# Optimization experiments

Hardware: AMD Instinct MI355X
Metric: run time of the kernel (lower is better)

Reference implementation:

```python
import jax, jax.numpy as jnp
import numpy as np

IN_C, OUT_C = 128, 256
KH, KW = 3, 3
STRIDE = (1, 1)
PAD = (1, 1)


def setup_inputs() -> dict:
    key = jax.random.key(0)
    kx, kw = jax.random.split(key)
    x = jax.random.normal(kx, (32, IN_C, 56, 56), dtype=jnp.float32)
    k = 1.0 / (IN_C * KH * KW)
    weight = (2.0 * jax.random.uniform(kw, (OUT_C, IN_C, KH, KW), dtype=jnp.float32) - 1.0) * (k ** 0.5)
    return {"x": x, "weight": weight}


def reference(x, weight):
    # Equivalent to the as_strided broadcast-multiply-sum: a plain 2D cross-correlation
    # (no bias), NCHW input, OIHW weight, stride (1,1), padding (1,1).
    return jax.lax.conv_general_dilated(
        x, weight,
        window_strides=STRIDE,
        padding=[(PAD[0], PAD[0]), (PAD[1], PAD[1])],
        dimension_numbers=("NCHW", "OIHW", "NCHW"),
    )
```

## Files before the change

### kernel.cpp

```cpp
#include <hip/hip_runtime.h>

typedef __attribute__((ext_vector_type(8))) short short8;
typedef __attribute__((ext_vector_type(4))) float floatx4;

#define IN_C 128
#define OUT_C 256
#define NB 32
#define HW 56
#define S_PER_N (HW * HW)
#define M_TOTAL (NB * S_PER_N)
#define PH 58
#define PW 66
#define XN_ELEMS (NB * PH * PW * IN_C)
#define WT_ELEMS (9 * OUT_C * IN_C)
#define XF_BLOCKS (PH * NB)
#define WF_BLOCKS (WT_ELEMS / 256)

__device__ __forceinline__ unsigned short f2bf(float f) {
    unsigned int u = __builtin_bit_cast(unsigned int, f);
    u = (u + 0x7FFFu + ((u >> 16) & 1u)) >> 16;
    return (unsigned short)u;
}

__device__ __forceinline__ void gld_lds16(const unsigned short* g, unsigned short* l) {
    __builtin_amdgcn_global_load_lds(
        (const __attribute__((address_space(1))) unsigned int*)g,
        (__attribute__((address_space(3))) unsigned int*)l, 16, 0, 0);
}

__global__ void xform_all(const float* __restrict__ x, const float* __restrict__ w,
                          unsigned short* __restrict__ xn, unsigned short* __restrict__ wt) {
    const int bid = blockIdx.x;
    const int tid = threadIdx.x;

    if (bid >= XF_BLOCKS) {
        const int idx = (bid - XF_BLOCKS) * 256 + tid;
        const int ic  = idx & 127;
        const int oc  = (idx >> 7) & 255;
        const int khw = idx >> 15;
        wt[idx] = f2bf(w[(oc * IN_C + ic) * 9 + khw]);
        return;
    }

    const int ihp = bid % PH;
    const int n   = bid / PH;
    unsigned int* __restrict__ row32 =
        (unsigned int*)(xn + (size_t)(n * PH + ihp) * PW * IN_C);
    const int WORDS = PW * IN_C / 2;

    if (ihp == 0 || ihp == PH - 1) {
        for (int i = tid; i < WORDS; i += 256) row32[i] = 0u;
        return;
    }
    if (tid < 128) {
        int p = (tid >> 6) * (PW - 1);
        row32[p * 64 + (tid & 63)] = 0u;
    }
    const int ih = ihp - 1;
    const float* __restrict__ xrow = x + (size_t)n * IN_C * S_PER_N + (size_t)ih * HW;
#pragma unroll
    for (int t = 0; t < 4; ++t) {
        const int item = tid + t * 256;
        if (item >= 64 * 14) break;
        const int icw  = item & 63;
        const int pix4 = item >> 6;
        const float4 v0 = *(const float4*)(xrow + (size_t)(2 * icw)     * S_PER_N + pix4 * 4);
        const float4 v1 = *(const float4*)(xrow + (size_t)(2 * icw + 1) * S_PER_N + pix4 * 4);
        unsigned int* o = row32 + (pix4 * 4 + 1) * 64 + icw;
        o[0]   = (unsigned int)f2bf(v0.x) | ((unsigned int)f2bf(v1.x) << 16);
        o[64]  = (unsigned int)f2bf(v0.y) | ((unsigned int)f2bf(v1.y) << 16);
        o[128] = (unsigned int)f2bf(v0.z) | ((unsigned int)f2bf(v1.z) << 16);
        o[192] = (unsigned int)f2bf(v0.w) | ((unsigned int)f2bf(v1.w) << 16);
    }
}

__global__ void __launch_bounds__(256, 3)
conv_mfma(const unsigned short* __restrict__ xn,
          const unsigned short* __restrict__ wt,
          float* __restrict__ out) {
    const int tid  = threadIdx.x;
    const int lane = tid & 63;
    const int wv   = tid >> 6;
    const int l15  = lane & 15;
    const int quad = lane >> 4;

    const int bx0 = blockIdx.x;
    const int bx  = (bx0 & 7) * 196 + (bx0 >> 3);
    const int tile_oc = bx & 1;
    const int tile_m  = bx >> 1;

    const int s_blk  = tile_m * 128;
    const int oc_blk = tile_oc * 128;
    const int s0  = s_blk + (wv & 1) * 64;
    const int oc0 = oc_blk + (wv >> 1) * 64;

    __shared__ unsigned short A_lds[128 * 64];
    __shared__ unsigned short B_lds[128 * 64];

    const int srow = tid >> 3;
    const int sic  = ((tid & 7) ^ (srow & 7)) * 8;

    const unsigned short* a_g[4];
    const unsigned short* b_g[4];
#pragma unroll
    for (int q = 0; q < 4; ++q) {
        int row = q * 32 + srow;
        a_g[q] = wt + (size_t)(oc_blk + row) * IN_C + sic;
        int sg = s_blk + row;
        int n  = sg / S_PER_N;
        int r  = sg % S_PER_N;
        int oh = r / HW, ow = r % HW;
        b_g[q] = xn + (size_t)((n * PH + oh) * PW + ow) * IN_C + sic;
    }
    unsigned short* a_l = A_lds + tid * 8;
    unsigned short* b_l = B_lds + tid * 8;

    const int fr7 = l15 & 7;
    int afo[4], bfo[4];
#pragma unroll
    for (int i = 0; i < 4; ++i)
        afo[i] = ((wv >> 1) * 64 + i * 16 + l15) * 64 + ((quad ^ fr7) * 8);
#pragma unroll
    for (int j = 0; j < 4; ++j)
        bfo[j] = ((wv & 1) * 64 + j * 16 + l15) * 64 + ((quad ^ fr7) * 8);

    floatx4 acc[4][4];
#pragma unroll
    for (int i = 0; i < 4; ++i)
#pragma unroll
        for (int j = 0; j < 4; ++j) acc[i][j] = (floatx4){0.f, 0.f, 0.f, 0.f};

#pragma unroll
    for (int khw = 0; khw < 9; ++khw) {
        const int xo = ((khw / 3) * PW + (khw % 3)) * IN_C;
        const int wo = khw * OUT_C * IN_C;
#pragma unroll
        for (int h = 0; h < 2; ++h) {
            const int ic0 = h * 64;
            __syncthreads();
#pragma unroll
            for (int q = 0; q < 4; ++q) {
                gld_lds16(a_g[q] + wo + ic0, a_l + q * 2048);
                gld_lds16(b_g[q] + xo + ic0, b_l + q * 2048);
            }
            __syncthreads();

#pragma unroll
            for (int kk = 0; kk < 2; ++kk) {
                const int ko = kk * 32;
                short8 a[4], b[4];
#pragma unroll
                for (int i = 0; i < 4; ++i) a[i] = *(const short8*)(A_lds + (afo[i] ^ ko));
#pragma unroll
                for (int j = 0; j < 4; ++j) b[j] = *(const short8*)(B_lds + (bfo[j] ^ ko));
#pragma unroll
                for (int i = 0; i < 4; ++i)
#pragma unroll
                    for (int j = 0; j < 4; ++j)
                        acc[i][j] = __builtin_amdgcn_mfma_f32_16x16x32_bf16(
                            a[i], b[j], acc[i][j], 0, 0, 0);
            }
        }
    }

#pragma unroll
    for (int j = 0; j < 4; ++j) {
        int s_glob = s0 + j * 16 + l15;
        int n = s_glob / S_PER_N;
        int s = s_glob % S_PER_N;
        float* obase = out + (size_t)n * OUT_C * S_PER_N + s;
#pragma unroll
        for (int i = 0; i < 4; ++i) {
            int oc = oc0 + i * 16 + quad * 4;
#pragma unroll
            for (int r = 0; r < 4; ++r)
                obase[(size_t)(oc + r) * S_PER_N] = acc[i][j][r];
        }
    }
}

extern "C" void kernel_launch(void* const* d_in, const int* in_sizes, int n_in,
                              void* d_out, int out_size, void* d_ws, size_t ws_size,
                              hipStream_t stream) {
    const float* x = (const float*)d_in[0];
    const float* w = (const float*)d_in[1];
    float* out = (float*)d_out;

    unsigned short* xn = (unsigned short*)d_ws;
    unsigned short* wt = xn + XN_ELEMS;

    xform_all<<<XF_BLOCKS + WF_BLOCKS, 256, 0, stream>>>(x, w, xn, wt);
    conv_mfma<<<(M_TOTAL / 128) * 2, 256, 0, stream>>>(xn, wt, out);
}
```

Before: 203.6 us.

## Enlarge conv GEMM tile to all 256 output channels per block

Each block now computes all 256 output channels for 128 spatial positions instead of splitting channels across two blocks. Each wave holds an 8x4 grid of MFMA accumulators, so the input patch loaded into LDS is reused across twice as many channels and is no longer fetched by two separate blocks. The cost is double the accumulator registers and a larger A tile in LDS. Occupancy drops (launch bounds 3 to 2 blocks per CU), there are half as many blocks, and the swizzle over 784 blocks changes.

```diff
diff --git a/kernel.cpp b/kernel.cpp
--- a/kernel.cpp
+++ b/kernel.cpp
@@ -74,59 +74,55 @@
     }
 }
 
-__global__ void __launch_bounds__(256, 3)
+__global__ void __launch_bounds__(256, 2)
 conv_mfma(const unsigned short* __restrict__ xn,
           const unsigned short* __restrict__ wt,
           float* __restrict__ out) {
     const int tid  = threadIdx.x;
     const int lane = tid & 63;
     const int wv   = tid >> 6;
+    const int ws   = wv & 1;
+    const int wo_  = wv >> 1;
     const int l15  = lane & 15;
     const int quad = lane >> 4;
+    const int fr7  = l15 & 7;
 
-    const int bx0 = blockIdx.x;
-    const int bx  = (bx0 & 7) * 196 + (bx0 >> 3);
-    const int tile_oc = bx & 1;
-    const int tile_m  = bx >> 1;
+    const int bx0    = blockIdx.x;
+    const int tile_m = (bx0 & 7) * 98 + (bx0 >> 3);
+    const int s_blk  = tile_m * 128;
 
-    const int s_blk  = tile_m * 128;
-    const int oc_blk = tile_oc * 128;
-    const int s0  = s_blk + (wv & 1) * 64;
-    const int oc0 = oc_blk + (wv >> 1) * 64;
-
-    __shared__ unsigned short A_lds[128 * 64];
+    __shared__ unsigned short A_lds[256 * 64];
     __shared__ unsigned short B_lds[128 * 64];
 
     const int srow = tid >> 3;
     const int sic  = ((tid & 7) ^ (srow & 7)) * 8;
 
-    const unsigned short* a_g[4];
+    const unsigned short* a_g[8];
     const unsigned short* b_g[4];
 #pragma unroll
-    for (int q = 0; q < 4; ++q) {
-        int row = q * 32 + srow;
-        a_g[q] = wt + (size_t)(oc_blk + row) * IN_C + sic;
-        int sg = s_blk + row;
+    for (int g = 0; g < 8; ++g)
+        a_g[g] = wt + (size_t)(g * 32 + srow) * IN_C + sic;
+#pragma unroll
+    for (int g = 0; g < 4; ++g) {
+        int sg = s_blk + g * 32 + srow;
         int n  = sg / S_PER_N;
         int r  = sg % S_PER_N;
         int oh = r / HW, ow = r % HW;
-        b_g[q] = xn + (size_t)((n * PH + oh) * PW + ow) * IN_C + sic;
+        b_g[g] = xn + (size_t)((n * PH + oh) * PW + ow) * IN_C + sic;
     }
-    unsigned short* a_l = A_lds + tid * 8;
-    unsigned short* b_l = B_lds + tid * 8;
 
-    const int fr7 = l15 & 7;
-    int afo[4], bfo[4];
+    const int slot = (quad ^ fr7) * 8;
+    int afo[8], bfo[4];
 #pragma unroll
-    for (int i = 0; i < 4; ++i)
-        afo[i] = ((wv >> 1) * 64 + i * 16 + l15) * 64 + ((quad ^ fr7) * 8);
+    for (int i = 0; i < 8; ++i)
+        afo[i] = (wo_ * 128 + i * 16 + l15) * 64 + slot;
 #pragma unroll
     for (int j = 0; j < 4; ++j)
-        bfo[j] = ((wv & 1) * 64 + j * 16 + l15) * 64 + ((quad ^ fr7) * 8);
+        bfo[j] = (ws * 64 + j * 16 + l15) * 64 + slot;
 
-    floatx4 acc[4][4];
+    floatx4 acc[8][4];
 #pragma unroll
-    for (int i = 0; i < 4; ++i)
+    for (int i = 0; i < 8; ++i)
 #pragma unroll
         for (int j = 0; j < 4; ++j) acc[i][j] = (floatx4){0.f, 0.f, 0.f, 0.f};
 
@@ -139,22 +135,23 @@
             const int ic0 = h * 64;
             __syncthreads();
 #pragma unroll
-            for (int q = 0; q < 4; ++q) {
-                gld_lds16(a_g[q] + wo + ic0, a_l + q * 2048);
-                gld_lds16(b_g[q] + xo + ic0, b_l + q * 2048);
-            }
+            for (int g = 0; g < 8; ++g)
+                gld_lds16(a_g[g] + wo + ic0, A_lds + g * 2048 + tid * 8);
+#pragma unroll
+            for (int g = 0; g < 4; ++g)
+                gld_lds16(b_g[g] + xo + ic0, B_lds + g * 2048 + tid * 8);
             __syncthreads();
 
 #pragma unroll
             for (int kk = 0; kk < 2; ++kk) {
                 const int ko = kk * 32;
-                short8 a[4], b[4];
+                short8 a[8], b[4];
 #pragma unroll
-                for (int i = 0; i < 4; ++i) a[i] = *(const short8*)(A_lds + (afo[i] ^ ko));
+                for (int i = 0; i < 8; ++i) a[i] = *(const short8*)(A_lds + (afo[i] ^ ko));
 #pragma unroll
                 for (int j = 0; j < 4; ++j) b[j] = *(const short8*)(B_lds + (bfo[j] ^ ko));
 #pragma unroll
-                for (int i = 0; i < 4; ++i)
+                for (int i = 0; i < 8; ++i)
 #pragma unroll
                     for (int j = 0; j < 4; ++j)
                         acc[i][j] = __builtin_amdgcn_mfma_f32_16x16x32_bf16(
@@ -163,6 +160,8 @@
         }
     }
 
+    const int s0  = s_blk + ws * 64;
+    const int oc0 = wo_ * 128;
 #pragma unroll
     for (int j = 0; j < 4; ++j) {
         int s_glob = s0 + j * 16 + l15;
@@ -170,7 +169,7 @@
         int s = s_glob % S_PER_N;
         float* obase = out + (size_t)n * OUT_C * S_PER_N + s;
 #pragma unroll
-        for (int i = 0; i < 4; ++i) {
+        for (int i = 0; i < 8; ++i) {
             int oc = oc0 + i * 16 + quad * 4;
 #pragma unroll
             for (int r = 0; r < 4; ++r)
@@ -190,5 +189,5 @@
     unsigned short* wt = xn + XN_ELEMS;
 
     xform_all<<<XF_BLOCKS + WF_BLOCKS, 256, 0, stream>>>(x, w, xn, wt);
-    conv_mfma<<<(M_TOTAL / 128) * 2, 256, 0, stream>>>(xn, wt, out);
+    conv_mfma<<<M_TOTAL / 128, 256, 0, stream>>>(xn, wt, out);
 }
```

New measurement: 209.0 us. 1.03x slower.

## Double-buffer LDS tiles to overlap global loads with MFMA compute

Applied to the files above, without the earlier changes.

Splits A and B shared tiles into two buffers and prefetches the next K-slice with direct global-to-LDS loads while MFMAs consume the current one. One barrier per step replaces the previous two. LDS use doubles to 64 KB per block and launch bounds drop to 2 blocks per CU, which lowers occupancy. The barrier placement after the waitcnt must still stop the writes to the next buffer from racing with reads of the old one.

```diff
diff --git a/kernel.cpp b/kernel.cpp
--- a/kernel.cpp
+++ b/kernel.cpp
@@ -74,7 +74,7 @@
     }
 }
 
-__global__ void __launch_bounds__(256, 3)
+__global__ void __launch_bounds__(256, 2)
 conv_mfma(const unsigned short* __restrict__ xn,
           const unsigned short* __restrict__ wt,
           float* __restrict__ out) {
@@ -83,6 +83,7 @@
     const int wv   = tid >> 6;
     const int l15  = lane & 15;
     const int quad = lane >> 4;
+    const int fr7  = l15 & 7;
 
     const int bx0 = blockIdx.x;
     const int bx  = (bx0 & 7) * 196 + (bx0 >> 3);
@@ -94,8 +95,8 @@
     const int s0  = s_blk + (wv & 1) * 64;
     const int oc0 = oc_blk + (wv >> 1) * 64;
 
-    __shared__ unsigned short A_lds[128 * 64];
-    __shared__ unsigned short B_lds[128 * 64];
+    __shared__ unsigned short A_lds[2][128 * 64];
+    __shared__ unsigned short B_lds[2][128 * 64];
 
     const int srow = tid >> 3;
     const int sic  = ((tid & 7) ^ (srow & 7)) * 8;
@@ -112,17 +113,15 @@
         int oh = r / HW, ow = r % HW;
         b_g[q] = xn + (size_t)((n * PH + oh) * PW + ow) * IN_C + sic;
     }
-    unsigned short* a_l = A_lds + tid * 8;
-    unsigned short* b_l = B_lds + tid * 8;
-
-    const int fr7 = l15 & 7;
+
+    const int slot = (quad ^ fr7) * 8;
     int afo[4], bfo[4];
 #pragma unroll
     for (int i = 0; i < 4; ++i)
-        afo[i] = ((wv >> 1) * 64 + i * 16 + l15) * 64 + ((quad ^ fr7) * 8);
+        afo[i] = ((wv >> 1) * 64 + i * 16 + l15) * 64 + slot;
 #pragma unroll
     for (int j = 0; j < 4; ++j)
-        bfo[j] = ((wv & 1) * 64 + j * 16 + l15) * 64 + ((quad ^ fr7) * 8);
+        bfo[j] = ((wv & 1) * 64 + j * 16 + l15) * 64 + slot;
 
     floatx4 acc[4][4];
 #pragma unroll
@@ -131,36 +130,44 @@
         for (int j = 0; j < 4; ++j) acc[i][j] = (floatx4){0.f, 0.f, 0.f, 0.f};
 
 #pragma unroll
-    for (int khw = 0; khw < 9; ++khw) {
-        const int xo = ((khw / 3) * PW + (khw % 3)) * IN_C;
-        const int wo = khw * OUT_C * IN_C;
-#pragma unroll
-        for (int h = 0; h < 2; ++h) {
-            const int ic0 = h * 64;
-            __syncthreads();
+    for (int q = 0; q < 4; ++q) {
+        gld_lds16(a_g[q], &A_lds[0][q * 2048 + tid * 8]);
+        gld_lds16(b_g[q], &B_lds[0][q * 2048 + tid * 8]);
+    }
+    asm volatile("s_waitcnt vmcnt(0)" ::: "memory");
+    __builtin_amdgcn_s_barrier();
+
+#pragma unroll
+    for (int t = 0; t < 18; ++t) {
+        const int c = t & 1;
+        if (t < 17) {
+            const int tn   = t + 1;
+            const int khwn = tn >> 1;
+            const int awo  = khwn * (OUT_C * IN_C) + (tn & 1) * 64;
+            const int bxo  = ((khwn / 3) * PW + (khwn % 3)) * IN_C + (tn & 1) * 64;
 #pragma unroll
             for (int q = 0; q < 4; ++q) {
-                gld_lds16(a_g[q] + wo + ic0, a_l + q * 2048);
-                gld_lds16(b_g[q] + xo + ic0, b_l + q * 2048);
-            }
-            __syncthreads();
-
-#pragma unroll
-            for (int kk = 0; kk < 2; ++kk) {
-                const int ko = kk * 32;
-                short8 a[4], b[4];
-#pragma unroll
-                for (int i = 0; i < 4; ++i) a[i] = *(const short8*)(A_lds + (afo[i] ^ ko));
-#pragma unroll
-                for (int j = 0; j < 4; ++j) b[j] = *(const short8*)(B_lds + (bfo[j] ^ ko));
-#pragma unroll
-                for (int i = 0; i < 4; ++i)
-#pragma unroll
-                    for (int j = 0; j < 4; ++j)
-                        acc[i][j] = __builtin_amdgcn_mfma_f32_16x16x32_bf16(
-                            a[i], b[j], acc[i][j], 0, 0, 0);
+                gld_lds16(a_g[q] + awo, &A_lds[1 - c][q * 2048 + tid * 8]);
+                gld_lds16(b_g[q] + bxo, &B_lds[1 - c][q * 2048 + tid * 8]);
             }
         }
+#pragma unroll
+        for (int kk = 0; kk < 2; ++kk) {
+            const int ko = kk * 32;
+            short8 a[4], b[4];
+#pragma unroll
+            for (int i = 0; i < 4; ++i) a[i] = *(const short8*)(&A_lds[c][0] + (afo[i] ^ ko));
+#pragma unroll
+            for (int j = 0; j < 4; ++j) b[j] = *(const short8*)(&B_lds[c][0] + (bfo[j] ^ ko));
+#pragma unroll
+            for (int i = 0; i < 4; ++i)
+#pragma unroll
+                for (int j = 0; j < 4; ++j)
+                    acc[i][j] = __builtin_amdgcn_mfma_f32_16x16x32_bf16(
+                        a[i], b[j], acc[i][j], 0, 0, 0);
+        }
+        asm volatile("s_waitcnt vmcnt(0)" ::: "memory");
+        __builtin_amdgcn_s_barrier();
     }
 
 #pragma unroll
```

Result: slower. 209.3 us (+2.8%).
